# Kernel optimization log

Hardware: AMD Instinct MI355X
Metric: run time of the kernel (lower is better)

Reference implementation:

```python
import jax, jax.numpy as jnp
import numpy as np

LN_EPS = 1e-5


def _forward(x, conv_w, conv_b, ln_w, ln_b, in_proj_w, in_proj_b, out_proj_w, out_proj_b):
    # x: (1, duration, dimensions)
    B, Dur, Dim = x.shape
    xt = jnp.transpose(x, (0, 2, 1))  # (1, Dim, Dur) -> Conv1d NCH layout
    branches = []
    for b in range(Dur):  # structural loop over the 32 conv branches (kernel size k=b+1)
        k = b + 1
        L = Dur - b  # output length duration - k + 1
        w = conv_w[b, :, :, :k]  # (Dim_out, Dim_in, k); padded taps beyond k unused
        y = jax.lax.conv_general_dilated(
            xt, w, window_strides=(1,), padding='VALID',
            dimension_numbers=('NCH', 'OIH', 'NCH'))  # (1, Dim, L)
        y = y + conv_b[b][None, :, None]
        y = jax.nn.gelu(y, approximate=False)  # torch nn.GELU default is exact erf form
        # LayerNorm(normalized_shape=[1, Dim, L]) with batch==1 normalizes the whole tensor
        mu = jnp.mean(y)
        var = jnp.var(y)  # biased, matching torch LayerNorm
        y = (y - mu) * jax.lax.rsqrt(var + LN_EPS)
        y = y * ln_w[b, :, :L][None] + ln_b[b, :, :L][None]
        branches.append(y)  # dropout is identity at inference (p=0.0)
    xc = jnp.concatenate(branches, axis=2)  # (1, Dim, T), T = Dur*(Dur+1)//2
    T = xc.shape[2]

    # nn.MultiheadAttention(embed_dim=T, num_heads=T), batch_first=False: input (L=1, N=Dim, E=T).
    # With seq_len==1, softmax over the single key is exactly 1, so attention output is
    # out_proj(v_proj(value)). value_i = x[:, i, :] broadcast over N, so every batch row of
    # output_i equals out_proj(v_proj(xc[0, i])). Summing over i (the feature loop):
    Wv = in_proj_w[2 * T:]          # (T, T) value slice of in_proj
    bv = in_proj_b[2 * T:]          # (T,)
    V = xc[0] @ Wv.T + bv           # (Dim, T): row i is v-proj of feature i
    S = V.sum(axis=0) @ out_proj_w.T + Dim * out_proj_b  # (T,)  sum over the Dim-term loop
    xa = jnp.broadcast_to(S[None, None, :], (1, Dim, T))  # identical rows, as in torch

    # x.unfold(2, Dur, 4*Dur).mean(-1)
    step = 4 * Dur
    n_w = (T - Dur) // step + 1
    idx = jnp.arange(n_w)[:, None] * step + jnp.arange(Dur)[None, :]  # (n_w, Dur)
    pooled = xa[:, :, idx].mean(-1)  # (1, Dim, n_w)
    return jnp.transpose(pooled, (0, 2, 1))  # (1, n_w, Dim)


def setup_inputs() -> dict:
    key = jax.random.key(0)
    ks = jax.random.split(key, 6)
    Dur, Dim = 32, 256
    T = Dur * (Dur + 1) // 2  # 528
    x = jax.random.normal(ks[0], (1, Dur, Dim), jnp.float32)
    conv_w = jax.random.normal(ks[1], (Dur, Dim, Dim, Dur), jnp.float32) * 0.02  # padded kernel bank
    conv_b = jax.random.normal(ks[2], (Dur, Dim), jnp.float32) * 0.02
    ln_w = jnp.ones((Dur, Dim, Dur), jnp.float32)   # branch b uses [:, :, :Dur-b]
    ln_b = jnp.zeros((Dur, Dim, Dur), jnp.float32)
    in_proj_w = jax.random.normal(ks[3], (3 * T, T), jnp.float32) * 0.02
    in_proj_b = jnp.zeros((3 * T,), jnp.float32)
    out_proj_w = jax.random.normal(ks[4], (T, T), jnp.float32) * 0.02
    out_proj_b = jnp.zeros((T,), jnp.float32)
    return {"x": x, "conv_w": conv_w, "conv_b": conv_b, "ln_w": ln_w, "ln_b": ln_b,
            "in_proj_w": in_proj_w, "in_proj_b": in_proj_b,
            "out_proj_w": out_proj_w, "out_proj_b": out_proj_b}


def reference(x, conv_w, conv_b, ln_w, ln_b, in_proj_w, in_proj_b, out_proj_w, out_proj_b):
    return _forward(x, conv_w, conv_b, ln_w, ln_b, in_proj_w, in_proj_b, out_proj_w, out_proj_b)
```

## Files before the change

kernel.cpp:

```cpp
#include <hip/hip_runtime.h>
#include <math.h>

#define DUR 32
#define DIM 256
#define TT  528

#define WS_BSUM 0
#define WS_BSQ  32
#define WS_CY   64
#define WS_CW   592
#define WS_CB   1120
#define WS_S    1648
#define WS_S2   2176
#define WS_ZERO_FLOATS 1648

__device__ __forceinline__ float gelu_exact(float v) {
    return 0.5f * v * (1.0f + erff(v * 0.70710678118654752f));
}

template<int K4>
__device__ __forceinline__ void conv_body(
    const int bb, const int o0, const int tid,
    const float* __restrict__ x, const float* __restrict__ W,
    const float* __restrict__ convb, const float* __restrict__ lnw,
    const float* __restrict__ lnb, float* __restrict__ ws,
    char* __restrict__ smem, float (* __restrict__ red)[4][32],
    float (* __restrict__ epi)[4][32], float (* __restrict__ sred)[2])
{
    constexpr bool DB  = (K4 < 8);
    constexpr int BUFB = 256 * 16 * K4;
    const int k = bb + 1;
    const int L = 32 - bb;
    const int wave = tid >> 6;
    const int lane = tid & 63;

    float xv[35];
#pragma unroll
    for (int tau = 0; tau < 32; ++tau) xv[tau] = x[tau * DIM + tid];
    xv[32] = 0.f; xv[33] = 0.f; xv[34] = 0.f;

    const float* Wb = W + (size_t)bb * (DIM * DIM * DUR) + (size_t)o0 * (DIM * DUR);

    float4 wreg[K4];
    auto issue = [&](int oo) {
#pragma unroll
        for (int r = 0; r < K4; ++r) {
            const int e = r * 256 + tid;
            wreg[r] = *(const float4*)(Wb + (size_t)oo * (DIM * DUR)
                                        + (e / K4) * 32 + (e % K4) * 4);
        }
    };
    auto stage = [&](int p) {
#pragma unroll
        for (int r = 0; r < K4; ++r) {
            const int e = r * 256 + tid;
            const int n = e / K4, m = e % K4;
            *(float4*)(smem + p * BUFB + (n * K4 + (m + n) % K4) * 16) = wreg[r];
        }
    };

    float cy = 0.f, cw = 0.f, cbv = 0.f, s1 = 0.f, s2 = 0.f;

    auto epilogue = [&](int j) {
        const int o = o0 + j;
        float g = 0.f;
        if (lane < L) {
            const float y = red[j & 1][0][lane] + red[j & 1][1][lane]
                          + red[j & 1][2][lane] + red[j & 1][3][lane]
                          + convb[bb * DIM + o];
            g = gelu_exact(y);
            const float lw = lnw[((size_t)(bb * DIM + o)) * DUR + lane];
            const float lb = lnb[((size_t)(bb * DIM + o)) * DUR + lane];
            cy += g * lw; cw += lw; cbv += lb;
        }
        s1 += g; s2 += g * g;
    };

    issue(0);
#pragma unroll
    for (int oo = 0; oo < 8; ++oo) {
        const int p = DB ? (oo & 1) : 0;
        if (!DB && oo > 0) __syncthreads();
        stage(p);
        __syncthreads();
        if (oo < 7) issue(oo + 1);

        if (oo > 0 && wave == ((oo - 1) & 3)) epilogue(oo - 1);

        float acc[32];
#pragma unroll
        for (int t = 0; t < 32; ++t) acc[t] = 0.f;

        const char* myrow = smem + p * BUFB + tid * (16 * K4);
#pragma unroll
        for (int m = 0; m < K4; ++m) {
            float4 w4 = *(const float4*)(myrow + ((m + tid) % K4) * 16);
            if (4 * m + 0 >= k) w4.x = 0.f;
            if (4 * m + 1 >= k) w4.y = 0.f;
            if (4 * m + 2 >= k) w4.z = 0.f;
            if (4 * m + 3 >= k) w4.w = 0.f;
#pragma unroll
            for (int t = 0; t < 32; ++t) {
                if (t < L) {
                    acc[t] = fmaf(xv[t + 4*m + 0], w4.x, acc[t]);
                    acc[t] = fmaf(xv[t + 4*m + 1], w4.y, acc[t]);
                    acc[t] = fmaf(xv[t + 4*m + 2], w4.z, acc[t]);
                    acc[t] = fmaf(xv[t + 4*m + 3], w4.w, acc[t]);
                }
            }
        }

#pragma unroll
        for (int t = 0; t < 32; ++t) {
            if (t < L) {
                float v = acc[t];
                v += __shfl_down(v, 32, 64);
                v += __shfl_down(v, 16, 64);
                v += __shfl_down(v, 8, 64);
                v += __shfl_down(v, 4, 64);
                v += __shfl_down(v, 2, 64);
                v += __shfl_down(v, 1, 64);
                if (lane == 0) red[oo & 1][wave][t] = v;
            }
        }
    }
    __syncthreads();
    if (wave == 3) epilogue(7);

    if (lane < 32) {
        epi[0][wave][lane] = cy;
        epi[1][wave][lane] = cw;
        epi[2][wave][lane] = cbv;
    }
    {
        float a = s1, b2 = s2;
        a += __shfl_down(a, 32, 64);  b2 += __shfl_down(b2, 32, 64);
        a += __shfl_down(a, 16, 64);  b2 += __shfl_down(b2, 16, 64);
        a += __shfl_down(a, 8, 64);   b2 += __shfl_down(b2, 8, 64);
        a += __shfl_down(a, 4, 64);   b2 += __shfl_down(b2, 4, 64);
        a += __shfl_down(a, 2, 64);   b2 += __shfl_down(b2, 2, 64);
        a += __shfl_down(a, 1, 64);   b2 += __shfl_down(b2, 1, 64);
        if (lane == 0) { sred[wave][0] = a; sred[wave][1] = b2; }
    }
    __syncthreads();
    if (wave == 0 && lane < L) {
        const int tg = bb * 32 - (bb * (bb - 1)) / 2 + lane;
        atomicAdd(ws + WS_CY + tg, epi[0][0][lane] + epi[0][1][lane] + epi[0][2][lane] + epi[0][3][lane]);
        atomicAdd(ws + WS_CW + tg, epi[1][0][lane] + epi[1][1][lane] + epi[1][2][lane] + epi[1][3][lane]);
        atomicAdd(ws + WS_CB + tg, epi[2][0][lane] + epi[2][1][lane] + epi[2][2][lane] + epi[2][3][lane]);
    }
    if (tid == 0) {
        atomicAdd(ws + WS_BSUM + bb, sred[0][0] + sred[1][0] + sred[2][0] + sred[3][0]);
        atomicAdd(ws + WS_BSQ  + bb, sred[0][1] + sred[1][1] + sred[2][1] + sred[3][1]);
    }
}

__global__ __launch_bounds__(256) void conv_kernel(
    const float* __restrict__ x, const float* __restrict__ W,
    const float* __restrict__ convb, const float* __restrict__ lnw,
    const float* __restrict__ lnb, float* ws)
{
    __shared__ char  smem[57344];
    __shared__ float red[2][4][32];
    __shared__ float epi[3][4][32];
    __shared__ float sred[4][2];

    const int bid = blockIdx.x;
    const int bb  = 31 - (bid & 31);
    const int o0  = (bid >> 5) * 8;
    const int tid = threadIdx.x;

    switch (bb >> 2) {
        case 0: conv_body<1>(bb, o0, tid, x, W, convb, lnw, lnb, ws, smem, red, epi, sred); break;
        case 1: conv_body<2>(bb, o0, tid, x, W, convb, lnw, lnb, ws, smem, red, epi, sred); break;
        case 2: conv_body<3>(bb, o0, tid, x, W, convb, lnw, lnb, ws, smem, red, epi, sred); break;
        case 3: conv_body<4>(bb, o0, tid, x, W, convb, lnw, lnb, ws, smem, red, epi, sred); break;
        case 4: conv_body<5>(bb, o0, tid, x, W, convb, lnw, lnb, ws, smem, red, epi, sred); break;
        case 5: conv_body<6>(bb, o0, tid, x, W, convb, lnw, lnb, ws, smem, red, epi, sred); break;
        case 6: conv_body<7>(bb, o0, tid, x, W, convb, lnw, lnb, ws, smem, red, epi, sred); break;
        default: conv_body<8>(bb, o0, tid, x, W, convb, lnw, lnb, ws, smem, red, epi, sred); break;
    }
}

__global__ __launch_bounds__(256) void proj1_kernel(
    float* ws, const float* __restrict__ in_proj_w,
    const float* __restrict__ in_proj_b)
{
    __shared__ float cc[TT];
    __shared__ float mu_s[32], r_s[32];
    __shared__ int map[TT];
    const int n = threadIdx.x;
    if (n < 32) {
        const int Lb = 32 - n;
        const float cnt = 256.f * (float)Lb;
        const float mu = ws[WS_BSUM + n] / cnt;
        const float var = ws[WS_BSQ + n] / cnt - mu * mu;
        mu_s[n] = mu;
        r_s[n] = rsqrtf(var + 1e-5f);
        const int off = n * 32 - (n * (n - 1)) / 2;
        for (int t = 0; t < Lb; ++t) map[off + t] = n;
    }
    __syncthreads();
    for (int t = n; t < TT; t += 256) {
        const int b = map[t];
        cc[t] = (ws[WS_CY + t] - mu_s[b] * ws[WS_CW + t]) * r_s[b] + ws[WS_CB + t];
    }
    __syncthreads();
    const int wave = n >> 6, lane = n & 63;
    const int row = blockIdx.x * 4 + wave;
    const float* Wr = in_proj_w + (size_t)(2 * TT + row) * TT;
    float a = 0.f;
    for (int t = lane; t < TT; t += 64) a = fmaf(Wr[t], cc[t], a);
    a += __shfl_down(a, 32, 64);
    a += __shfl_down(a, 16, 64);
    a += __shfl_down(a, 8, 64);
    a += __shfl_down(a, 4, 64);
    a += __shfl_down(a, 2, 64);
    a += __shfl_down(a, 1, 64);
    if (lane == 0) ws[WS_S + row] = a + 256.f * in_proj_b[2 * TT + row];
}

__global__ __launch_bounds__(256) void proj2a_kernel(
    float* ws, const float* __restrict__ out_proj_w,
    const float* __restrict__ out_proj_b)
{
    const int i = blockIdx.x;
    const int u = (i >> 5) * 128 + (i & 31);
    const int n = threadIdx.x;
    const int wave = n >> 6, lane = n & 63;
    const float* Or = out_proj_w + (size_t)u * TT;
    float a = 0.f;
    for (int t = n; t < TT; t += 256) a = fmaf(Or[t], ws[WS_S + t], a);
    a += __shfl_down(a, 32, 64);
    a += __shfl_down(a, 16, 64);
    a += __shfl_down(a, 8, 64);
    a += __shfl_down(a, 4, 64);
    a += __shfl_down(a, 2, 64);
    a += __shfl_down(a, 1, 64);
    __shared__ float r4[4];
    if (lane == 0) r4[wave] = a;
    __syncthreads();
    if (n == 0) ws[WS_S2 + i] = r4[0] + r4[1] + r4[2] + r4[3] + 256.f * out_proj_b[u];
}

__global__ __launch_bounds__(256) void proj2b_kernel(
    const float* __restrict__ ws, float* __restrict__ out)
{
    const int n = threadIdx.x;
    __shared__ float mv;
    if (n < 64) {
        float v = (n < 32) ? ws[WS_S2 + blockIdx.x * 32 + n] : 0.f;
        v += __shfl_down(v, 16, 64);
        v += __shfl_down(v, 8, 64);
        v += __shfl_down(v, 4, 64);
        v += __shfl_down(v, 2, 64);
        v += __shfl_down(v, 1, 64);
        if (n == 0) mv = v * (1.0f / 32.0f);
    }
    __syncthreads();
    out[blockIdx.x * 256 + n] = mv;
}

extern "C" void kernel_launch(void* const* d_in, const int* in_sizes, int n_in,
                              void* d_out, int out_size, void* d_ws, size_t ws_size,
                              hipStream_t stream)
{
    const float* x   = (const float*)d_in[0];
    const float* W   = (const float*)d_in[1];
    const float* cb  = (const float*)d_in[2];
    const float* lnw = (const float*)d_in[3];
    const float* lnb = (const float*)d_in[4];
    const float* ipw = (const float*)d_in[5];
    const float* ipb = (const float*)d_in[6];
    const float* opw = (const float*)d_in[7];
    const float* opb = (const float*)d_in[8];
    float* ws  = (float*)d_ws;
    float* out = (float*)d_out;

    hipMemsetAsync(ws, 0, WS_ZERO_FLOATS * sizeof(float), stream);
    conv_kernel<<<1024, 256, 0, stream>>>(x, W, cb, lnw, lnb, ws);
    proj1_kernel<<<132, 256, 0, stream>>>(ws, ipw, ipb);
    proj2a_kernel<<<128, 256, 0, stream>>>(ws, opw, opb);
    proj2b_kernel<<<4, 256, 0, stream>>>(ws, out);
}
```

Before: 445.9 us.

## Stream conv weights into LDS via direct global_load_lds with double buffering

Weight tiles for each output-channel group now go straight from global memory into LDS with 16-byte global_load_lds. This replaces the old path of loading into registers and then storing to shared memory. Source offsets are pre-permuted so the swizzled LDS layout is preserved. Double buffering is now always on, and the accumulator and reduction loops are bounded by a compile-time per-K4 maximum length. A launch-bounds hint for two blocks per CU is added. The aim is to cut VGPR pressure and staging instructions and to overlap weight transfer with compute. The risk is that correct ordering now depends on the barrier waiting for the asynchronous LDS writes.

```diff
diff --git a/kernel.cpp b/kernel.cpp
--- a/kernel.cpp
+++ b/kernel.cpp
@@ -1,5 +1,6 @@
 #include <hip/hip_runtime.h>
 #include <math.h>
+#include <stdint.h>
 
 #define DUR 32
 #define DIM 256
@@ -18,21 +19,26 @@
     return 0.5f * v * (1.0f + erff(v * 0.70710678118654752f));
 }
 
+__device__ __forceinline__ void gl_lds16(const float* g, float* l) {
+    __builtin_amdgcn_global_load_lds(
+        (const __attribute__((address_space(1))) uint32_t*)g,
+        (__attribute__((address_space(3))) uint32_t*)l, 16, 0, 0);
+}
+
 template<int K4>
 __device__ __forceinline__ void conv_body(
     const int bb, const int o0, const int tid,
     const float* __restrict__ x, const float* __restrict__ W,
     const float* __restrict__ convb, const float* __restrict__ lnw,
     const float* __restrict__ lnb, float* __restrict__ ws,
-    char* __restrict__ smem, float (* __restrict__ red)[4][32],
+    float* __restrict__ smem, float (* __restrict__ red)[4][32],
     float (* __restrict__ epi)[4][32], float (* __restrict__ sred)[2])
 {
-    constexpr bool DB  = (K4 < 8);
-    constexpr int BUFB = 256 * 16 * K4;
+    constexpr int Lmax = 36 - 4 * K4;
+    constexpr int BUFF = 256 * K4 * 4;
     const int k = bb + 1;
     const int L = 32 - bb;
-    const int wave = tid >> 6;
-    const int lane = tid & 63;
+    const int wave = tid >> 6, lane = tid & 63;
 
     float xv[35];
 #pragma unroll
@@ -41,66 +47,41 @@
 
     const float* Wb = W + (size_t)bb * (DIM * DIM * DUR) + (size_t)o0 * (DIM * DUR);
 
-    float4 wreg[K4];
-    auto issue = [&](int oo) {
+    int srcoff[K4];
+#pragma unroll
+    for (int r = 0; r < K4; ++r) {
+        const int s = r * 256 + tid;
+        const int n = s / K4;
+        const int j = s - n * K4;
+        int m = j - (n % K4); if (m < 0) m += K4;
+        srcoff[r] = n * 32 + m * 4;
+    }
+
+    auto issue = [&](int oo, int p) {
+        float* base = smem + p * BUFF;
 #pragma unroll
         for (int r = 0; r < K4; ++r) {
-            const int e = r * 256 + tid;
-            wreg[r] = *(const float4*)(Wb + (size_t)oo * (DIM * DUR)
-                                        + (e / K4) * 32 + (e % K4) * 4);
+            float* l = base + (r * 256 + wave * 64) * 4;
+            const float* g = Wb + (size_t)oo * 8192 + srcoff[r];
+            gl_lds16(g, l);
         }
     };
-    auto stage = [&](int p) {
-#pragma unroll
-        for (int r = 0; r < K4; ++r) {
-            const int e = r * 256 + tid;
-            const int n = e / K4, m = e % K4;
-            *(float4*)(smem + p * BUFB + (n * K4 + (m + n) % K4) * 16) = wreg[r];
-        }
-    };
-
-    float cy = 0.f, cw = 0.f, cbv = 0.f, s1 = 0.f, s2 = 0.f;
-
-    auto epilogue = [&](int j) {
-        const int o = o0 + j;
-        float g = 0.f;
-        if (lane < L) {
-            const float y = red[j & 1][0][lane] + red[j & 1][1][lane]
-                          + red[j & 1][2][lane] + red[j & 1][3][lane]
-                          + convb[bb * DIM + o];
-            g = gelu_exact(y);
-            const float lw = lnw[((size_t)(bb * DIM + o)) * DUR + lane];
-            const float lb = lnb[((size_t)(bb * DIM + o)) * DUR + lane];
-            cy += g * lw; cw += lw; cbv += lb;
-        }
-        s1 += g; s2 += g * g;
-    };
-
-    issue(0);
-#pragma unroll
-    for (int oo = 0; oo < 8; ++oo) {
-        const int p = DB ? (oo & 1) : 0;
-        if (!DB && oo > 0) __syncthreads();
-        stage(p);
-        __syncthreads();
-        if (oo < 7) issue(oo + 1);
-
-        if (oo > 0 && wave == ((oo - 1) & 3)) epilogue(oo - 1);
-
-        float acc[32];
-#pragma unroll
-        for (int t = 0; t < 32; ++t) acc[t] = 0.f;
-
-        const char* myrow = smem + p * BUFB + tid * (16 * K4);
+
+    auto compute = [&](int p) {
+        float acc[Lmax];
+#pragma unroll
+        for (int t = 0; t < Lmax; ++t) acc[t] = 0.f;
+        const float* myrow = smem + p * BUFF + tid * (K4 * 4);
 #pragma unroll
         for (int m = 0; m < K4; ++m) {
-            float4 w4 = *(const float4*)(myrow + ((m + tid) % K4) * 16);
+            const int slot = (m + tid) % K4;
+            float4 w4 = *(const float4*)(myrow + slot * 4);
             if (4 * m + 0 >= k) w4.x = 0.f;
             if (4 * m + 1 >= k) w4.y = 0.f;
             if (4 * m + 2 >= k) w4.z = 0.f;
             if (4 * m + 3 >= k) w4.w = 0.f;
 #pragma unroll
-            for (int t = 0; t < 32; ++t) {
+            for (int t = 0; t < Lmax; ++t) {
                 if (t < L) {
                     acc[t] = fmaf(xv[t + 4*m + 0], w4.x, acc[t]);
                     acc[t] = fmaf(xv[t + 4*m + 1], w4.y, acc[t]);
@@ -109,9 +90,8 @@
                 }
             }
         }
-
-#pragma unroll
-        for (int t = 0; t < 32; ++t) {
+#pragma unroll
+        for (int t = 0; t < Lmax; ++t) {
             if (t < L) {
                 float v = acc[t];
                 v += __shfl_down(v, 32, 64);
@@ -120,9 +100,36 @@
                 v += __shfl_down(v, 4, 64);
                 v += __shfl_down(v, 2, 64);
                 v += __shfl_down(v, 1, 64);
-                if (lane == 0) red[oo & 1][wave][t] = v;
+                if (lane == 0) red[p][wave][t] = v;
             }
         }
+    };
+
+    float cy = 0.f, cw = 0.f, cbv = 0.f, s1 = 0.f, s2 = 0.f;
+
+    auto epilogue = [&](int j) {
+        const int o = o0 + j;
+        float g = 0.f;
+        if (lane < L) {
+            const int q = j & 1;
+            const float y = red[q][0][lane] + red[q][1][lane]
+                          + red[q][2][lane] + red[q][3][lane]
+                          + convb[bb * DIM + o];
+            g = gelu_exact(y);
+            const float lw = lnw[((size_t)(bb * DIM + o)) * DUR + lane];
+            const float lb = lnb[((size_t)(bb * DIM + o)) * DUR + lane];
+            cy += g * lw; cw += lw; cbv += lb;
+        }
+        s1 += g; s2 += g * g;
+    };
+
+    issue(0, 0);
+#pragma unroll
+    for (int oo = 0; oo < 8; ++oo) {
+        __syncthreads();
+        if (oo < 7) issue(oo + 1, (oo + 1) & 1);
+        if (oo > 0 && wave == ((oo - 1) & 3)) epilogue(oo - 1);
+        compute(oo & 1);
     }
     __syncthreads();
     if (wave == 3) epilogue(7);
@@ -155,12 +162,12 @@
     }
 }
 
-__global__ __launch_bounds__(256) void conv_kernel(
+__global__ __launch_bounds__(256, 2) void conv_kernel(
     const float* __restrict__ x, const float* __restrict__ W,
     const float* __restrict__ convb, const float* __restrict__ lnw,
     const float* __restrict__ lnb, float* ws)
 {
-    __shared__ char  smem[57344];
+    __shared__ float smem[2 * 256 * 8 * 4];
     __shared__ float red[2][4][32];
     __shared__ float epi[3][4][32];
     __shared__ float sred[4][2];
```

After: 450.3 us. About the same (+1.0%).
